# Optimization experiments

Measured on AMD Instinct MI355X. Metric: run time of the kernel, lower is better.

## Reference

```python
import jax, jax.numpy as jnp
from jax import lax
import numpy as np

EPS = 1e-6
DN = ('NCHW', 'OIHW', 'NCHW')  # conv dimension numbers matching torch F.conv2d


def setup_inputs() -> dict:
    key = jax.random.key(0)
    kx, ky = jax.random.split(key)
    B, C, H, W = 16, 3, 512, 512
    x = jax.random.normal(kx, (B, C, H, W), dtype=jnp.float32)
    y = jax.random.normal(ky, (B, C, H, W), dtype=jnp.float32)
    return {"x": x, "y": y}


def _box_smooth(v):
    # 7x7 uniform kernel repeated over 3 input channels -> 1 output channel,
    # every tap weighted 1/49 (matches kernel.repeat(1,3,1,1) in torch).
    k = jnp.full((1, v.shape[1], 7, 7), 1.0 / 49.0, dtype=v.dtype)
    return lax.conv_general_dilated(v, k, window_strides=(1, 1),
                                    padding=[(3, 3), (3, 3)],
                                    dimension_numbers=DN)


def reference(x, y):
    # conv is linear, so conv(x) - conv(y) == conv(x - y); avoids one conv pass
    diff = _box_smooth(x - y)           # [B, 1, H, W]
    return jnp.mean(jnp.sqrt(diff * diff + EPS))  # scalar Charbonnier loss
```

## Files before the change

kernel.cpp:

```cpp
#include <hip/hip_runtime.h>
#include <math.h>


namespace {
constexpr int kB = 16, kC = 3, kH = 512, kW = 512;
constexpr int ROWS = 8;
constexpr int BANDS_PER_IMG = kH / ROWS;
constexpr int NBANDS = kB * BANDS_PER_IMG;
constexpr int WPB = 2;
constexpr int NT = WPB * 64;
constexpr int NB = NBANDS / WPB;
constexpr float EPS = 1e-6f;
}

struct RowRegs { float4 a[6]; float4 b[6]; };

__device__ __forceinline__ void issue_row(RowRegs& R,
                                          const float* __restrict__ xb,
                                          const float* __restrict__ yb,
                                          int rclamp, int c0) {
  const size_t HW = (size_t)kH * kW;
  const float* px = xb + (size_t)rclamp * kW + c0;
  const float* py = yb + (size_t)rclamp * kW + c0;
#pragma unroll
  for (int ch = 0; ch < 3; ++ch) {
    R.a[ch]     = *(const float4*)(px + ch * HW);
    R.b[ch]     = *(const float4*)(px + ch * HW + 4);
    R.a[3 + ch] = *(const float4*)(py + ch * HW);
    R.b[3 + ch] = *(const float4*)(py + ch * HW + 4);
  }
}

__global__ __launch_bounds__(NT, 1)
void charbox_kernel(const float* __restrict__ x, const float* __restrict__ y,
                    float* __restrict__ out) {
  __shared__ float red[WPB];

  const int tid  = threadIdx.x;
  const int lane = tid & 63;
  const int wid  = tid >> 6;
  const int band = blockIdx.x * WPB + wid;
  const int b    = band >> 6;
  const int r0   = (band & 63) * ROWS;
  const size_t HW = (size_t)kH * kW;
  const float* xb = x + (size_t)b * kC * HW;
  const float* yb = y + (size_t)b * kC * HW;
  const int c0 = lane * 8;
  const int laneL = (lane + 63) & 63;
  const int laneR = (lane + 1) & 63;

  float ring[7][8];
  float v[8];
#pragma unroll
  for (int k = 0; k < 7; ++k)
#pragma unroll
    for (int j = 0; j < 8; ++j) ring[k][j] = 0.f;
#pragma unroll
  for (int j = 0; j < 8; ++j) v[j] = 0.f;
  float acc = 0.f;

  RowRegs buf[2];
  issue_row(buf[0], xb, yb, max(r0 - 3, 0), c0);

#pragma unroll
  for (int it = 0; it < ROWS + 6; ++it) {
    if (it + 1 < ROWS + 6) {
      const int rn = r0 - 3 + it + 1;
      issue_row(buf[(it + 1) & 1], xb, yb, min(max(rn, 0), kH - 1), c0);
    }
    const RowRegs& R = buf[it & 1];
    const int r = r0 - 3 + it;
    const bool valid = (r >= 0) & (r < kH);

    float z[8];
    if (valid) {
      z[0] = (R.a[0].x - R.a[3].x) + (R.a[1].x - R.a[4].x) + (R.a[2].x - R.a[5].x);
      z[1] = (R.a[0].y - R.a[3].y) + (R.a[1].y - R.a[4].y) + (R.a[2].y - R.a[5].y);
      z[2] = (R.a[0].z - R.a[3].z) + (R.a[1].z - R.a[4].z) + (R.a[2].z - R.a[5].z);
      z[3] = (R.a[0].w - R.a[3].w) + (R.a[1].w - R.a[4].w) + (R.a[2].w - R.a[5].w);
      z[4] = (R.b[0].x - R.b[3].x) + (R.b[1].x - R.b[4].x) + (R.b[2].x - R.b[5].x);
      z[5] = (R.b[0].y - R.b[3].y) + (R.b[1].y - R.b[4].y) + (R.b[2].y - R.b[5].y);
      z[6] = (R.b[0].z - R.b[3].z) + (R.b[1].z - R.b[4].z) + (R.b[2].z - R.b[5].z);
      z[7] = (R.b[0].w - R.b[3].w) + (R.b[1].w - R.b[4].w) + (R.b[2].w - R.b[5].w);
    } else {
#pragma unroll
      for (int j = 0; j < 8; ++j) z[j] = 0.f;
    }

    const float l5 = __shfl(z[5], laneL, 64);
    const float l6 = __shfl(z[6], laneL, 64);
    const float l7 = __shfl(z[7], laneL, 64);
    const float g0 = __shfl(z[0], laneR, 64);
    const float g1 = __shfl(z[1], laneR, 64);
    const float g2 = __shfl(z[2], laneR, 64);
    float e[14];
    e[0] = lane ? l5 : 0.f;
    e[1] = lane ? l6 : 0.f;
    e[2] = lane ? l7 : 0.f;
#pragma unroll
    for (int j = 0; j < 8; ++j) e[3 + j] = z[j];
    e[11] = (lane < 63) ? g0 : 0.f;
    e[12] = (lane < 63) ? g1 : 0.f;
    e[13] = (lane < 63) ? g2 : 0.f;

    float h[8];
    float s = ((e[0] + e[1]) + (e[2] + e[3])) + ((e[4] + e[5]) + e[6]);
    h[0] = s;
#pragma unroll
    for (int j = 1; j < 8; ++j) {
      s += e[j + 6] - e[j - 1];
      h[j] = s;
    }

    const int slot = it % 7;
#pragma unroll
    for (int j = 0; j < 8; ++j) {
      v[j] += h[j] - ring[slot][j];
      ring[slot][j] = h[j];
    }

    if (it >= 6) {
#pragma unroll
      for (int j = 0; j < 8; ++j) {
        const float d = v[j] * (1.0f / 49.0f);
        acc += sqrtf(fmaf(d, d, EPS));
      }
    }
  }

#pragma unroll
  for (int off = 32; off > 0; off >>= 1) acc += __shfl_down(acc, off, 64);
  if (lane == 0) red[wid] = acc;
  __syncthreads();
  if (tid == 0) {
    const float ssum = red[0] + red[1];
    atomicAdd(out, ssum * (1.0f / ((float)kB * (float)kH * (float)kW)));
  }
}

extern "C" void kernel_launch(void* const* d_in, const int* in_sizes, int n_in,
                              void* d_out, int out_size, void* d_ws, size_t ws_size,
                              hipStream_t stream) {
  const float* x = (const float*)d_in[0];
  const float* y = (const float*)d_in[1];
  float* out = (float*)d_out;

  charbox_kernel<<<NB, NT, 0, stream>>>(x, y, out);
}
```

Before: 126.2 us.

## Shrink row bands to two outputs per wave and swizzle blocks across XCDs

Each wave now produces 2 output rows instead of 8, quadrupling the number of waves, and each block holds 4 waves. The 7-slot ring buffer is replaced by two direct vertical accumulators. Block indices are remapped so that consecutive bands land on the same XCD for L2 locality. This raises parallelism and cuts register use, but each band rereads 6 halo rows for every 2 output rows, so global and L2 read traffic goes up several-fold.

```diff
diff --git a/kernel.cpp b/kernel.cpp
--- a/kernel.cpp
+++ b/kernel.cpp
@@ -4,12 +4,14 @@
 
 namespace {
 constexpr int kB = 16, kC = 3, kH = 512, kW = 512;
-constexpr int ROWS = 8;
+constexpr int ROWS = 2;
+constexpr int INROWS = ROWS + 6;
 constexpr int BANDS_PER_IMG = kH / ROWS;
 constexpr int NBANDS = kB * BANDS_PER_IMG;
-constexpr int WPB = 2;
+constexpr int WPB = 4;
 constexpr int NT = WPB * 64;
 constexpr int NB = NBANDS / WPB;
+constexpr int NXCD = 8;
 constexpr float EPS = 1e-6f;
 }
 
@@ -39,9 +41,10 @@
   const int tid  = threadIdx.x;
   const int lane = tid & 63;
   const int wid  = tid >> 6;
-  const int band = blockIdx.x * WPB + wid;
-  const int b    = band >> 6;
-  const int r0   = (band & 63) * ROWS;
+  const int swz  = (blockIdx.x % NXCD) * (NB / NXCD) + blockIdx.x / NXCD;
+  const int band = swz * WPB + wid;
+  const int b    = band >> 8;
+  const int r0   = (band & 255) * ROWS;
   const size_t HW = (size_t)kH * kW;
   const float* xb = x + (size_t)b * kC * HW;
   const float* yb = y + (size_t)b * kC * HW;
@@ -49,22 +52,17 @@
   const int laneL = (lane + 63) & 63;
   const int laneR = (lane + 1) & 63;
 
-  float ring[7][8];
-  float v[8];
+  float v0[8], v1[8];
 #pragma unroll
-  for (int k = 0; k < 7; ++k)
-#pragma unroll
-    for (int j = 0; j < 8; ++j) ring[k][j] = 0.f;
-#pragma unroll
-  for (int j = 0; j < 8; ++j) v[j] = 0.f;
+  for (int j = 0; j < 8; ++j) { v0[j] = 0.f; v1[j] = 0.f; }
   float acc = 0.f;
 
   RowRegs buf[2];
   issue_row(buf[0], xb, yb, max(r0 - 3, 0), c0);
 
 #pragma unroll
-  for (int it = 0; it < ROWS + 6; ++it) {
-    if (it + 1 < ROWS + 6) {
+  for (int it = 0; it < INROWS; ++it) {
+    if (it + 1 < INROWS) {
       const int rn = r0 - 3 + it + 1;
       issue_row(buf[(it + 1) & 1], xb, yb, min(max(rn, 0), kH - 1), c0);
     }
@@ -112,20 +110,22 @@
       h[j] = s;
     }
 
-    const int slot = it % 7;
+    if (it <= 6) {
 #pragma unroll
-    for (int j = 0; j < 8; ++j) {
-      v[j] += h[j] - ring[slot][j];
-      ring[slot][j] = h[j];
+      for (int j = 0; j < 8; ++j) v0[j] += h[j];
     }
+    if (it >= 1) {
+#pragma unroll
+      for (int j = 0; j < 8; ++j) v1[j] += h[j];
+    }
+  }
 
-    if (it >= 6) {
 #pragma unroll
-      for (int j = 0; j < 8; ++j) {
-        const float d = v[j] * (1.0f / 49.0f);
-        acc += sqrtf(fmaf(d, d, EPS));
-      }
-    }
+  for (int j = 0; j < 8; ++j) {
+    const float d0 = v0[j] * (1.0f / 49.0f);
+    acc += sqrtf(fmaf(d0, d0, EPS));
+    const float d1 = v1[j] * (1.0f / 49.0f);
+    acc += sqrtf(fmaf(d1, d1, EPS));
   }
 
 #pragma unroll
@@ -133,7 +133,7 @@
   if (lane == 0) red[wid] = acc;
   __syncthreads();
   if (tid == 0) {
-    const float ssum = red[0] + red[1];
+    const float ssum = (red[0] + red[1]) + (red[2] + red[3]);
     atomicAdd(out, ssum * (1.0f / ((float)kB * (float)kH * (float)kW)));
   }
 }
```

New measurement: 127.3 us. Within noise of the previous version (+0.8%).
